# Performance work log

Measured on AMD Instinct MI355X. Metric: run time of the kernel, lower is better.

The kernel has to match this reference:

```python
import jax, jax.numpy as jnp
import numpy as np

N, E, C = 50000, 600000, 128
BN_EPS = 1e-5
NORM_EPS = 1e-12


def _edgeconv(x, src, dst, wa, ba, g, be, rm, rv, wb, bb):
    # PyG EdgeConv: message = MLP(concat(x_i, x_j - x_i)); aggr='add' at target i
    x_i = x[dst]                      # [E, C] target features
    x_j = x[src]                      # [E, C] source features
    m = jnp.concatenate([x_i, x_j - x_i], axis=-1)   # [E, 2C]
    m = jax.nn.relu(m @ wa.T + ba)                   # Linear(2C->C) + ReLU
    m = (m - rm) * (g * jax.lax.rsqrt(rv + BN_EPS)) + be  # BatchNorm1d (eval)
    m = m @ wb.T + bb                                # Linear(C->C)
    return jax.ops.segment_sum(m, dst, num_segments=x.shape[0])  # [N, C]


def _lin(k, fan_in, shape):
    bound = 1.0 / np.sqrt(fan_in)
    return jax.random.uniform(k, shape, jnp.float32, -bound, bound)


def setup_inputs() -> dict:
    key = jax.random.key(0)
    ks = jax.random.split(key, 16)
    inp = {
        "x": jax.random.normal(ks[0], (N, C), jnp.float32),
        "edge_index": jax.random.randint(ks[1], (2, E), 0, N, jnp.int64),
    }
    # layer 1 params
    inp["w1a"] = _lin(ks[2], 2 * C, (C, 2 * C)); inp["b1a"] = _lin(ks[3], 2 * C, (C,))
    inp["g1"] = jnp.ones((C,), jnp.float32) + 0.1 * jax.random.normal(ks[4], (C,))
    inp["be1"] = 0.1 * jax.random.normal(ks[5], (C,))
    inp["rm1"] = 0.1 * jax.random.normal(ks[6], (C,))
    inp["rv1"] = 0.5 + jax.random.uniform(ks[7], (C,))
    inp["w1b"] = _lin(ks[8], C, (C, C)); inp["b1b"] = _lin(ks[9], C, (C,))
    # layer 2 params
    inp["w2a"] = _lin(ks[10], 2 * C, (C, 2 * C)); inp["b2a"] = _lin(ks[11], 2 * C, (C,))
    inp["g2"] = jnp.ones((C,), jnp.float32) + 0.1 * jax.random.normal(ks[12], (C,))
    inp["be2"] = 0.1 * jax.random.normal(ks[13], (C,))
    inp["rm2"] = 0.1 * jax.random.normal(ks[14], (C,))
    inp["rv2"] = 0.5 + jax.random.uniform(ks[15], (C,))
    k2 = jax.random.split(ks[15], 2)
    inp["w2b"] = _lin(k2[0], C, (C, C)); inp["b2b"] = _lin(k2[1], C, (C,))
    return inp


def reference(x, edge_index, w1a, b1a, g1, be1, rm1, rv1, w1b, b1b,
              w2a, b2a, g2, be2, rm2, rv2, w2b, b2b):
    src, dst = edge_index[0], edge_index[1]
    # layer 1 (all but last): conv -> relu -> L2 normalize -> dropout(eval=identity)
    h = _edgeconv(x, src, dst, w1a, b1a, g1, be1, rm1, rv1, w1b, b1b)
    h = jax.nn.relu(h)
    h = h / jnp.maximum(jnp.linalg.norm(h, axis=-1, keepdims=True), NORM_EPS)
    # last layer: conv only
    return _edgeconv(h, src, dst, w2a, b2a, g2, be2, rm2, rv2, w2b, b2b)
```

## Files before the change

kernel.cpp:

```cpp
#include <hip/hip_runtime.h>

#define CCH 128
#define WPAD 136
typedef unsigned short ushort;
typedef __attribute__((ext_vector_type(8))) short bf16x8_t;
typedef __attribute__((ext_vector_type(4))) float f32x4;

union ABu { bf16x8_t v; ushort u[8]; uint4 q; };

__device__ __forceinline__ ushort f2b(float f) {
  union { float f; unsigned u; } v{f};
  unsigned r = v.u + 0x7fffu + ((v.u >> 16) & 1u);
  return (ushort)(r >> 16);
}
__device__ __forceinline__ float b2f(ushort s) {
  union { unsigned u; float f; } v{(unsigned)s << 16};
  return v.f;
}

__global__ __launch_bounds__(256) void k_pre(const float* __restrict__ w1a,
                                             const float* __restrict__ w1b,
                                             const float* __restrict__ w2a,
                                             const float* __restrict__ w2b,
                                             ushort* __restrict__ Wcat1, ushort* __restrict__ Wb1,
                                             ushort* __restrict__ Wcat2, ushort* __restrict__ Wb2,
                                             const void* __restrict__ ei, int* __restrict__ deg,
                                             int E) {
  const int b = blockIdx.x, t = threadIdx.x;
  if (b < 128) {
    int i = b * 256 + t;
    int c = i >> 7, k = i & 127;
    float v = (c < 128) ? w1a[c * 256 + k] - w1a[c * 256 + 128 + k]
                        : w1a[(c - 128) * 256 + 128 + k];
    Wcat1[i] = f2b(v);
    if (i < 16384) Wb1[i] = f2b(w1b[i]);
  } else if (b < 256) {
    int i = (b - 128) * 256 + t;
    int c = i >> 7, k = i & 127;
    float v = (c < 128) ? w2a[c * 256 + k] - w2a[c * 256 + 128 + k]
                        : w2a[(c - 128) * 256 + 128 + k];
    Wcat2[i] = f2b(v);
    if (i < 16384) Wb2[i] = f2b(w2b[i]);
  } else {
    __shared__ int nz;
    if (t == 0) nz = 0;
    __syncthreads();
    int e = (b - 256) * 256 + t;
    unsigned hi = (e < E) ? ((const unsigned*)ei)[2 * (size_t)e + 1] : 0u;
    if (hi) atomicAdd(&nz, 1);
    __syncthreads();
    bool i64 = (nz == 0);
    if (e < E) {
      int d = i64 ? (int)((const long long*)ei)[(size_t)E + e]
                  : ((const int*)ei)[(size_t)E + e];
      atomicAdd(&deg[d], 1);
    }
  }
}

__global__ __launch_bounds__(256) void k_scan1(const int* __restrict__ deg,
                                               int* __restrict__ bsum, int n) {
  __shared__ int s[256];
  int t = threadIdx.x, i = blockIdx.x * 256 + t;
  s[t] = (i < n) ? deg[i] : 0;
  __syncthreads();
  for (int off = 128; off > 0; off >>= 1) {
    if (t < off) s[t] += s[t + off];
    __syncthreads();
  }
  if (t == 0) bsum[blockIdx.x] = s[0];
}

__global__ __launch_bounds__(256) void k_rowptr(const int* __restrict__ deg,
                                                const int* __restrict__ bsum,
                                                int* __restrict__ rowptr,
                                                int* __restrict__ cnt,
                                                int n, int nb, int Etot) {
  __shared__ int s[256];
  const int t = threadIdx.x, b = blockIdx.x;
  s[t] = (t < nb && t < b) ? bsum[t] : 0;
  __syncthreads();
  for (int off = 128; off > 0; off >>= 1) {
    if (t < off) s[t] += s[t + off];
    __syncthreads();
  }
  int boffset = s[0];
  __syncthreads();
  int i = b * 256 + t;
  int v = (i < n) ? deg[i] : 0;
  s[t] = v; __syncthreads();
  for (int off = 1; off < 256; off <<= 1) {
    int tv = (t >= off) ? s[t - off] : 0;
    __syncthreads();
    s[t] += tv;
    __syncthreads();
  }
  if (i < n) {
    int rp = boffset + s[t] - v;
    rowptr[i] = rp;
    cnt[i] = rp;
  }
  if (b == gridDim.x - 1 && t == 0) rowptr[n] = Etot;
}

__device__ __forceinline__ void stage_w(const ushort* __restrict__ Wp,
                                        ushort* __restrict__ wlds, int t) {
  for (int i = t; i < 128 * 16; i += 256) {
    int row = i >> 4, ch = i & 15;
    *(uint4*)&wlds[row * WPAD + ch * 8] = *(const uint4*)&Wp[row * CCH + ch * 8];
  }
}

__device__ __forceinline__ void mfma8(const ABu a[4], const ushort* __restrict__ wlds,
                                      int ln, int quad, f32x4 acc[8]) {
#pragma unroll
  for (int s = 0; s < 8; ++s) acc[s] = (f32x4){0.f, 0.f, 0.f, 0.f};
#pragma unroll
  for (int s = 0; s < 8; ++s) {
#pragma unroll
    for (int kk = 0; kk < 4; ++kk) {
      ABu b;
      b.q = *(const uint4*)&wlds[(s * 16 + ln) * WPAD + kk * 32 + quad * 8];
      acc[s] = __builtin_amdgcn_mfma_f32_16x16x32_bf16(a[kk].v, b.v, acc[s], 0, 0, 0);
    }
  }
}

__device__ __forceinline__ void epi0(f32x4 acc[8], int rowb, int ln, int quad, int nN,
                                     const float* bias, int half, ushort* dst) {
#pragma unroll
  for (int s = 0; s < 8; ++s) {
    int col = s * 16 + ln;
    float bv = half ? 0.f : bias[col];
#pragma unroll
    for (int r = 0; r < 4; ++r) {
      int row = rowb + quad * 4 + r;
      if (row < nN) dst[(size_t)row * CCH + col] = f2b(acc[s][r] + bv);
    }
  }
}

__global__ __launch_bounds__(256) void k_mix(const float* __restrict__ X,
                                             const ushort* __restrict__ Wcat,
                                             const float* __restrict__ bias,
                                             ushort* __restrict__ A1,
                                             ushort* __restrict__ A2, int nN,
                                             const void* __restrict__ ei,
                                             int* __restrict__ cnt,
                                             int* __restrict__ esrc, int E, int gH) {
  __shared__ ushort wlds[128 * WPAD];
  const int t = threadIdx.x;
  if ((int)blockIdx.x >= 2 * gH) {
    int* nzp = (int*)wlds;
    if (t == 0) nzp[0] = 0;
    __syncthreads();
    int e = ((int)blockIdx.x - 2 * gH) * 256 + t;
    unsigned hi = (e < E) ? ((const unsigned*)ei)[2 * (size_t)e + 1] : 0u;
    if (hi) atomicAdd(nzp, 1);
    __syncthreads();
    bool i64 = (nzp[0] == 0);
    if (e < E) {
      int d, sv;
      if (i64) {
        sv = (int)((const long long*)ei)[(size_t)e];
        d  = (int)((const long long*)ei)[(size_t)E + e];
      } else {
        sv = ((const int*)ei)[(size_t)e];
        d  = ((const int*)ei)[(size_t)E + e];
      }
      int pos = atomicAdd(&cnt[d], 1);
      esrc[pos] = sv;
    }
    return;
  }
  const int half = (int)blockIdx.x >= gH;
  const int bx = half ? blockIdx.x - gH : blockIdx.x;
  stage_w(Wcat + (size_t)half * 128 * CCH, wlds, t);
  __syncthreads();
  const int wave = t >> 6, lane = t & 63;
  const int ln = lane & 15, quad = lane >> 4;
  const int rowb = bx * 128 + wave * 32;

  ABu a0[4], a1[4];
#pragma unroll
  for (int kk = 0; kk < 4; ++kk) {
    auto ldc = [&](int r, ABu& d) {
      if (r < nN) {
        const float* xp = X + (size_t)r * CCH + kk * 32 + quad * 8;
        float4 f0 = *(const float4*)xp;
        float4 f1 = *(const float4*)(xp + 4);
        d.u[0] = f2b(f0.x); d.u[1] = f2b(f0.y); d.u[2] = f2b(f0.z); d.u[3] = f2b(f0.w);
        d.u[4] = f2b(f1.x); d.u[5] = f2b(f1.y); d.u[6] = f2b(f1.z); d.u[7] = f2b(f1.w);
      } else d.q = make_uint4(0, 0, 0, 0);
    };
    ldc(rowb + ln, a0[kk]); ldc(rowb + 16 + ln, a1[kk]);
  }
  f32x4 acc[8];
  ushort* dst = half ? A2 : A1;
  mfma8(a0, wlds, ln, quad, acc);
  epi0(acc, rowb, ln, quad, nN, bias, half, dst);
  mfma8(a1, wlds, ln, quad, acc);
  epi0(acc, rowb + 16, ln, quad, nN, bias, half, dst);
}

template <int EPI>
__global__ __launch_bounds__(256) void k_gemm(const ushort* __restrict__ XB,
                                              const ushort* __restrict__ W,
                                              const float* __restrict__ bias,
                                              const int* __restrict__ deg,
                                              void* __restrict__ Y1,
                                              ushort* __restrict__ Y2, int nN) {
  __shared__ ushort wlds[128 * WPAD];
  const int t = threadIdx.x;
  const int half = (EPI == 0) ? blockIdx.y : 0;
  stage_w(W + (size_t)half * 128 * CCH, wlds, t);
  __syncthreads();
  const int wave = t >> 6, lane = t & 63;
  const int ln = lane & 15, quad = lane >> 4;
  const int rowb = blockIdx.x * 128 + wave * 32;

  ABu a0[4], a1[4];
#pragma unroll
  for (int kk = 0; kk < 4; ++kk) {
    int r0 = rowb + ln, r1 = rowb + 16 + ln;
    a0[kk].q = (r0 < nN) ? *(const uint4*)(XB + (size_t)r0 * CCH + kk * 32 + quad * 8)
                         : make_uint4(0, 0, 0, 0);
    a1[kk].q = (r1 < nN) ? *(const uint4*)(XB + (size_t)r1 * CCH + kk * 32 + quad * 8)
                         : make_uint4(0, 0, 0, 0);
  }
  f32x4 acc[8];

  if constexpr (EPI == 0) {
    ushort* dst = half ? Y2 : (ushort*)Y1;
    mfma8(a0, wlds, ln, quad, acc);
    epi0(acc, rowb, ln, quad, nN, bias, half, dst);
    mfma8(a1, wlds, ln, quad, acc);
    epi0(acc, rowb + 16, ln, quad, nN, bias, half, dst);
  } else if constexpr (EPI == 1) {
    ushort* H = (ushort*)Y1;
    float biasv[8];
#pragma unroll
    for (int s = 0; s < 8; ++s) biasv[s] = bias[s * 16 + ln];
    auto epi = [&](f32x4* ac, int rb) {
#pragma unroll
      for (int r = 0; r < 4; ++r) {
        int row = rb + quad * 4 + r;
        float dn = (row < nN) ? (float)deg[row] : 0.f;
        float vals[8];
        float ss = 0.f;
#pragma unroll
        for (int s = 0; s < 8; ++s) {
          float v = fmaxf(ac[s][r] + dn * biasv[s], 0.f);
          vals[s] = v;
          ss += v * v;
        }
        ss += __shfl_xor(ss, 1, 64);
        ss += __shfl_xor(ss, 2, 64);
        ss += __shfl_xor(ss, 4, 64);
        ss += __shfl_xor(ss, 8, 64);
        float inv = 1.0f / fmaxf(sqrtf(ss), 1e-12f);
        if (row < nN) {
#pragma unroll
          for (int s = 0; s < 8; ++s)
            H[(size_t)row * CCH + s * 16 + ln] = f2b(vals[s] * inv);
        }
      }
    };
    mfma8(a0, wlds, ln, quad, acc); epi(acc, rowb);
    mfma8(a1, wlds, ln, quad, acc); epi(acc, rowb + 16);
  } else {
    float* OUT = (float*)Y1;
    float biasv[8];
#pragma unroll
    for (int s = 0; s < 8; ++s) biasv[s] = bias[s * 16 + ln];
    auto epi = [&](f32x4* ac, int rb) {
#pragma unroll
      for (int r = 0; r < 4; ++r) {
        int row = rb + quad * 4 + r;
        if (row >= nN) continue;
        float dn = (float)deg[row];
#pragma unroll
        for (int s = 0; s < 8; ++s)
          OUT[(size_t)row * CCH + s * 16 + ln] = ac[s][r] + dn * biasv[s];
      }
    };
    mfma8(a0, wlds, ln, quad, acc); epi(acc, rowb);
    mfma8(a1, wlds, ln, quad, acc); epi(acc, rowb + 16);
  }
}

__global__ __launch_bounds__(256) void k_aggr(const ushort* __restrict__ A1,
                                              const ushort* __restrict__ A2,
                                              const int* __restrict__ rowptr,
                                              const int* __restrict__ esrc,
                                              const float* __restrict__ g,
                                              const float* __restrict__ be,
                                              const float* __restrict__ rm,
                                              const float* __restrict__ rv,
                                              ushort* __restrict__ M, int nNodes) {
  int node = blockIdx.x * 4 + (threadIdx.x >> 6);
  if (node >= nNodes) return;
  int lane = threadIdx.x & 63;
  int q = lane >> 4;
  int c = (lane & 15) * 8;

  uint4 aq = *(const uint4*)&A1[(size_t)node * CCH + c];
  float a[8] = {b2f((ushort)aq.x), b2f((ushort)(aq.x >> 16)),
                b2f((ushort)aq.y), b2f((ushort)(aq.y >> 16)),
                b2f((ushort)aq.z), b2f((ushort)(aq.z >> 16)),
                b2f((ushort)aq.w), b2f((ushort)(aq.w >> 16))};
  int r0 = rowptr[node], r1 = rowptr[node + 1];
  float s[8] = {0.f, 0.f, 0.f, 0.f, 0.f, 0.f, 0.f, 0.f};

  auto acc8 = [&](uint4 w) {
    const unsigned* p = (const unsigned*)&w;
#pragma unroll
    for (int j = 0; j < 4; ++j) {
      s[2*j]   += fmaxf(a[2*j]   + b2f((ushort)p[j]), 0.f);
      s[2*j+1] += fmaxf(a[2*j+1] + b2f((ushort)(p[j] >> 16)), 0.f);
    }
  };

  for (int base = r0; base < r1; base += 64) {
    int navail = r1 - base; if (navail > 64) navail = 64;
    int myi = (lane < navail) ? esrc[base + lane] : 0;
    int g4 = navail >> 2, tail = navail & 3;
    int j = 0;
    for (; j + 4 <= g4; j += 4) {
      int p0 = j * 4 + q;
      int i0 = __shfl(myi, p0, 64);
      int i1 = __shfl(myi, p0 + 4, 64);
      int i2 = __shfl(myi, p0 + 8, 64);
      int i3 = __shfl(myi, p0 + 12, 64);
      uint4 w0 = *(const uint4*)&A2[(size_t)i0 * CCH + c];
      uint4 w1 = *(const uint4*)&A2[(size_t)i1 * CCH + c];
      uint4 w2 = *(const uint4*)&A2[(size_t)i2 * CCH + c];
      uint4 w3 = *(const uint4*)&A2[(size_t)i3 * CCH + c];
      acc8(w0); acc8(w1); acc8(w2); acc8(w3);
    }
    for (; j < g4; ++j) {
      int i0 = __shfl(myi, j * 4 + q, 64);
      acc8(*(const uint4*)&A2[(size_t)i0 * CCH + c]);
    }
    int pt = g4 * 4 + q; if (pt > 63) pt = 63;
    int it = __shfl(myi, pt, 64);
    if (q < tail) acc8(*(const uint4*)&A2[(size_t)it * CCH + c]);
  }
#pragma unroll
  for (int j = 0; j < 8; ++j) {
    s[j] += __shfl_xor(s[j], 16, 64);
    s[j] += __shfl_xor(s[j], 32, 64);
  }

  if (q == 0) {
    float dn = (float)(r1 - r0);
    unsigned p[4];
#pragma unroll
    for (int j = 0; j < 4; ++j) {
      float sc0 = g[c + 2*j]     * rsqrtf(rv[c + 2*j]     + 1e-5f);
      float sc1 = g[c + 2*j + 1] * rsqrtf(rv[c + 2*j + 1] + 1e-5f);
      float o0 = sc0 * s[2*j]     + dn * (be[c + 2*j]     - rm[c + 2*j]     * sc0);
      float o1 = sc1 * s[2*j + 1] + dn * (be[c + 2*j + 1] - rm[c + 2*j + 1] * sc1);
      p[j] = (unsigned)f2b(o0) | ((unsigned)f2b(o1) << 16);
    }
    *(uint4*)&M[(size_t)node * CCH + c] = make_uint4(p[0], p[1], p[2], p[3]);
  }
}

extern "C" void kernel_launch(void* const* d_in, const int* in_sizes, int n_in,
                              void* d_out, int out_size, void* d_ws, size_t ws_size,
                              hipStream_t stream) {
  const float* x   = (const float*)d_in[0];
  const void*  ei  = d_in[1];
  const float* w1a = (const float*)d_in[2];
  const float* b1a = (const float*)d_in[3];
  const float* g1  = (const float*)d_in[4];
  const float* be1 = (const float*)d_in[5];
  const float* rm1 = (const float*)d_in[6];
  const float* rv1 = (const float*)d_in[7];
  const float* w1b = (const float*)d_in[8];
  const float* b1b = (const float*)d_in[9];
  const float* w2a = (const float*)d_in[10];
  const float* b2a = (const float*)d_in[11];
  const float* g2  = (const float*)d_in[12];
  const float* be2 = (const float*)d_in[13];
  const float* rm2 = (const float*)d_in[14];
  const float* rv2 = (const float*)d_in[15];
  const float* w2b = (const float*)d_in[16];
  const float* b2b = (const float*)d_in[17];

  const int N = in_sizes[0] / CCH;
  const int E = in_sizes[1] / 2;
  const size_t NC = (size_t)N * CCH;

  int* deg    = (int*)d_ws;
  int* cnt    = deg + N;
  int* rowptr = cnt + N;
  int* bsum   = rowptr + N + 1;
  int* esrc   = bsum + 256;
  uintptr_t pw = ((uintptr_t)(esrc + E) + 63) & ~(uintptr_t)63;
  ushort* Wcat1 = (ushort*)pw;
  ushort* Wcat2 = Wcat1 + 32768;
  ushort* Wb1   = Wcat2 + 32768;
  ushort* Wb2   = Wb1 + 16384;
  uintptr_t pb = ((uintptr_t)(Wb2 + 16384) + 63) & ~(uintptr_t)63;
  ushort* B0 = (ushort*)pb;
  ushort* B1 = B0 + NC;
  ushort* MB = B1 + NC;
  ushort* HB = MB + NC;

  const int gE  = (E + 255) / 256;
  const int gS  = (N + 255) / 256;
  const int gH  = (N + 127) / 128;
  const int gA  = (N + 3) / 4;

  hipMemsetAsync(deg, 0, sizeof(int) * (size_t)N, stream);
  k_pre<<<256 + gE, 256, 0, stream>>>(w1a, w1b, w2a, w2b,
                                      Wcat1, Wb1, Wcat2, Wb2, ei, deg, E);
  k_scan1<<<gS, 256, 0, stream>>>(deg, bsum, N);
  k_rowptr<<<gS, 256, 0, stream>>>(deg, bsum, rowptr, cnt, N, gS, E);
  k_mix<<<2 * gH + gE, 256, 0, stream>>>(x, Wcat1, b1a, B0, B1, N, ei, cnt, esrc, E, gH);

  k_aggr<<<gA, 256, 0, stream>>>(B0, B1, rowptr, esrc, g1, be1, rm1, rv1, MB, N);
  k_gemm<1><<<gH, 256, 0, stream>>>(MB, Wb1, b1b, deg, HB, nullptr, N);
  k_gemm<0><<<dim3(gH, 2), 256, 0, stream>>>(HB, Wcat2, b2a, deg, B0, B1, N);
  k_aggr<<<gA, 256, 0, stream>>>(B0, B1, rowptr, esrc, g2, be2, rm2, rv2, MB, N);
  k_gemm<2><<<gH, 256, 0, stream>>>(MB, Wb2, b2b, deg, d_out, nullptr, N);
}
```

Measured before the change: 305.1 us.

## Fuse edge scatter into mix GEMM blocks, use ballot for dtype check, smaller GEMM tiles

The edge-scatter work in k_mix moves out of its separate tail blocks: every GEMM block now also handles a contiguous chunk of edges after its matmul, so the grid shrinks to just the GEMM blocks. The shared-memory atomic plus barriers that detected int64 versus int32 indices is replaced by a wavefront ballot. The two node-level GEMMs with C=128 outputs (k_gemm<1> and k_gemm<2>) are templated on rows per block and launched with 64 rows per block, doubling block count to improve occupancy and load balance. The per-wave ballot assumes the dtype check over a wave's 64 edges is as reliable as the old block-wide check. The fused scatter lengthens each GEMM block's tail.

Measured after the change: 317.1 us. +3.9%, slower.

```diff
diff --git a/kernel.cpp b/kernel.cpp
--- a/kernel.cpp
+++ b/kernel.cpp
@@ -42,14 +42,9 @@
     Wcat2[i] = f2b(v);
     if (i < 16384) Wb2[i] = f2b(w2b[i]);
   } else {
-    __shared__ int nz;
-    if (t == 0) nz = 0;
-    __syncthreads();
     int e = (b - 256) * 256 + t;
     unsigned hi = (e < E) ? ((const unsigned*)ei)[2 * (size_t)e + 1] : 0u;
-    if (hi) atomicAdd(&nz, 1);
-    __syncthreads();
-    bool i64 = (nz == 0);
+    bool i64 = (__ballot(hi != 0u) == 0ull);
     if (e < E) {
       int d = i64 ? (int)((const long long*)ei)[(size_t)E + e]
                   : ((const int*)ei)[(size_t)E + e];
@@ -147,18 +142,43 @@
                                              ushort* __restrict__ A2, int nN,
                                              const void* __restrict__ ei,
                                              int* __restrict__ cnt,
-                                             int* __restrict__ esrc, int E, int gH) {
+                                             int* __restrict__ esrc, int E, int epb) {
   __shared__ ushort wlds[128 * WPAD];
   const int t = threadIdx.x;
-  if ((int)blockIdx.x >= 2 * gH) {
-    int* nzp = (int*)wlds;
-    if (t == 0) nzp[0] = 0;
-    __syncthreads();
-    int e = ((int)blockIdx.x - 2 * gH) * 256 + t;
+  const int half = blockIdx.x & 1;
+  const int bx = blockIdx.x >> 1;
+  stage_w(Wcat + (size_t)half * 128 * CCH, wlds, t);
+  __syncthreads();
+  const int wave = t >> 6, lane = t & 63;
+  const int ln = lane & 15, quad = lane >> 4;
+  const int rowb = bx * 128 + wave * 32;
+
+  ABu a0[4], a1[4];
+#pragma unroll
+  for (int kk = 0; kk < 4; ++kk) {
+    auto ldc = [&](int r, ABu& d) {
+      if (r < nN) {
+        const float* xp = X + (size_t)r * CCH + kk * 32 + quad * 8;
+        float4 f0 = *(const float4*)xp;
+        float4 f1 = *(const float4*)(xp + 4);
+        d.u[0] = f2b(f0.x); d.u[1] = f2b(f0.y); d.u[2] = f2b(f0.z); d.u[3] = f2b(f0.w);
+        d.u[4] = f2b(f1.x); d.u[5] = f2b(f1.y); d.u[6] = f2b(f1.z); d.u[7] = f2b(f1.w);
+      } else d.q = make_uint4(0, 0, 0, 0);
+    };
+    ldc(rowb + ln, a0[kk]); ldc(rowb + 16 + ln, a1[kk]);
+  }
+  f32x4 acc[8];
+  ushort* dst = half ? A2 : A1;
+  mfma8(a0, wlds, ln, quad, acc);
+  epi0(acc, rowb, ln, quad, nN, bias, half, dst);
+  mfma8(a1, wlds, ln, quad, acc);
+  epi0(acc, rowb + 16, ln, quad, nN, bias, half, dst);
+
+  const int ebase = blockIdx.x * epb;
+  for (int r = 0; r < epb; r += 256) {
+    int e = ebase + r + t;
     unsigned hi = (e < E) ? ((const unsigned*)ei)[2 * (size_t)e + 1] : 0u;
-    if (hi) atomicAdd(nzp, 1);
-    __syncthreads();
-    bool i64 = (nzp[0] == 0);
+    bool i64 = (__ballot(hi != 0u) == 0ull);
     if (e < E) {
       int d, sv;
       if (i64) {
@@ -171,39 +191,10 @@
       int pos = atomicAdd(&cnt[d], 1);
       esrc[pos] = sv;
     }
-    return;
-  }
-  const int half = (int)blockIdx.x >= gH;
-  const int bx = half ? blockIdx.x - gH : blockIdx.x;
-  stage_w(Wcat + (size_t)half * 128 * CCH, wlds, t);
-  __syncthreads();
-  const int wave = t >> 6, lane = t & 63;
-  const int ln = lane & 15, quad = lane >> 4;
-  const int rowb = bx * 128 + wave * 32;
-
-  ABu a0[4], a1[4];
-#pragma unroll
-  for (int kk = 0; kk < 4; ++kk) {
-    auto ldc = [&](int r, ABu& d) {
-      if (r < nN) {
-        const float* xp = X + (size_t)r * CCH + kk * 32 + quad * 8;
-        float4 f0 = *(const float4*)xp;
-        float4 f1 = *(const float4*)(xp + 4);
-        d.u[0] = f2b(f0.x); d.u[1] = f2b(f0.y); d.u[2] = f2b(f0.z); d.u[3] = f2b(f0.w);
-        d.u[4] = f2b(f1.x); d.u[5] = f2b(f1.y); d.u[6] = f2b(f1.z); d.u[7] = f2b(f1.w);
-      } else d.q = make_uint4(0, 0, 0, 0);
-    };
-    ldc(rowb + ln, a0[kk]); ldc(rowb + 16 + ln, a1[kk]);
-  }
-  f32x4 acc[8];
-  ushort* dst = half ? A2 : A1;
-  mfma8(a0, wlds, ln, quad, acc);
-  epi0(acc, rowb, ln, quad, nN, bias, half, dst);
-  mfma8(a1, wlds, ln, quad, acc);
-  epi0(acc, rowb + 16, ln, quad, nN, bias, half, dst);
-}
-
-template <int EPI>
+  }
+}
+
+template <int EPI, int ROWS>
 __global__ __launch_bounds__(256) void k_gemm(const ushort* __restrict__ XB,
                                               const ushort* __restrict__ W,
                                               const float* __restrict__ bias,
@@ -217,16 +208,20 @@
   __syncthreads();
   const int wave = t >> 6, lane = t & 63;
   const int ln = lane & 15, quad = lane >> 4;
-  const int rowb = blockIdx.x * 128 + wave * 32;
-
+  const int rowb = blockIdx.x * ROWS + wave * (ROWS / 4);
+
+  constexpr int NT = ROWS / 64;
   ABu a0[4], a1[4];
 #pragma unroll
   for (int kk = 0; kk < 4; ++kk) {
-    int r0 = rowb + ln, r1 = rowb + 16 + ln;
+    int r0 = rowb + ln;
     a0[kk].q = (r0 < nN) ? *(const uint4*)(XB + (size_t)r0 * CCH + kk * 32 + quad * 8)
                          : make_uint4(0, 0, 0, 0);
-    a1[kk].q = (r1 < nN) ? *(const uint4*)(XB + (size_t)r1 * CCH + kk * 32 + quad * 8)
-                         : make_uint4(0, 0, 0, 0);
+    if (NT == 2) {
+      int r1 = rowb + 16 + ln;
+      a1[kk].q = (r1 < nN) ? *(const uint4*)(XB + (size_t)r1 * CCH + kk * 32 + quad * 8)
+                           : make_uint4(0, 0, 0, 0);
+    }
   }
   f32x4 acc[8];
 
@@ -234,8 +229,10 @@
     ushort* dst = half ? Y2 : (ushort*)Y1;
     mfma8(a0, wlds, ln, quad, acc);
     epi0(acc, rowb, ln, quad, nN, bias, half, dst);
-    mfma8(a1, wlds, ln, quad, acc);
-    epi0(acc, rowb + 16, ln, quad, nN, bias, half, dst);
+    if (NT == 2) {
+      mfma8(a1, wlds, ln, quad, acc);
+      epi0(acc, rowb + 16, ln, quad, nN, bias, half, dst);
+    }
   } else if constexpr (EPI == 1) {
     ushort* H = (ushort*)Y1;
     float biasv[8];
@@ -267,7 +264,7 @@
       }
     };
     mfma8(a0, wlds, ln, quad, acc); epi(acc, rowb);
-    mfma8(a1, wlds, ln, quad, acc); epi(acc, rowb + 16);
+    if (NT == 2) { mfma8(a1, wlds, ln, quad, acc); epi(acc, rowb + 16); }
   } else {
     float* OUT = (float*)Y1;
     float biasv[8];
@@ -285,7 +282,7 @@
       }
     };
     mfma8(a0, wlds, ln, quad, acc); epi(acc, rowb);
-    mfma8(a1, wlds, ln, quad, acc); epi(acc, rowb + 16);
+    if (NT == 2) { mfma8(a1, wlds, ln, quad, acc); epi(acc, rowb + 16); }
   }
 }
 
@@ -412,18 +409,21 @@
   const int gE  = (E + 255) / 256;
   const int gS  = (N + 255) / 256;
   const int gH  = (N + 127) / 128;
+  const int gF  = (N + 63) / 64;
   const int gA  = (N + 3) / 4;
+  const int gM  = 2 * gH;
+  const int epb = (((E + gM - 1) / gM + 255) / 256) * 256;
 
   hipMemsetAsync(deg, 0, sizeof(int) * (size_t)N, stream);
   k_pre<<<256 + gE, 256, 0, stream>>>(w1a, w1b, w2a, w2b,
                                       Wcat1, Wb1, Wcat2, Wb2, ei, deg, E);
   k_scan1<<<gS, 256, 0, stream>>>(deg, bsum, N);
   k_rowptr<<<gS, 256, 0, stream>>>(deg, bsum, rowptr, cnt, N, gS, E);
-  k_mix<<<2 * gH + gE, 256, 0, stream>>>(x, Wcat1, b1a, B0, B1, N, ei, cnt, esrc, E, gH);
+  k_mix<<<gM, 256, 0, stream>>>(x, Wcat1, b1a, B0, B1, N, ei, cnt, esrc, E, epb);
 
   k_aggr<<<gA, 256, 0, stream>>>(B0, B1, rowptr, esrc, g1, be1, rm1, rv1, MB, N);
-  k_gemm<1><<<gH, 256, 0, stream>>>(MB, Wb1, b1b, deg, HB, nullptr, N);
-  k_gemm<0><<<dim3(gH, 2), 256, 0, stream>>>(HB, Wcat2, b2a, deg, B0, B1, N);
+  k_gemm<1, 64><<<gF, 256, 0, stream>>>(MB, Wb1, b1b, deg, HB, nullptr, N);
+  k_gemm<0, 128><<<dim3(gH, 2), 256, 0, stream>>>(HB, Wcat2, b2a, deg, B0, B1, N);
   k_aggr<<<gA, 256, 0, stream>>>(B0, B1, rowptr, esrc, g2, be2, rm2, rv2, MB, N);
-  k_gemm<2><<<gH, 256, 0, stream>>>(MB, Wb2, b2b, deg, d_out, nullptr, N);
-}
+  k_gemm<2, 64><<<gF, 256, 0, stream>>>(MB, Wb2, b2b, deg, d_out, nullptr, N);
+}
```
